# Performance work log

Hardware: AMD Instinct MI355X
Metric: run time of the kernel (lower is better)

Reference implementation:

```python
import jax, jax.numpy as jnp
import numpy as np

# Model dims
T0 = 2048      # tokens (batch*seq flattened)
D = 2048       # hidden_size
E = 256        # n_routed_experts
K = 8          # num_experts_per_tok
G = 8          # expert groups
EG = 32        # experts per group
R = 64         # tucker rank
I = 1408       # moe_intermediate_size


def setup_inputs() -> dict:
    key = jax.random.key(0)
    ks = jax.random.split(key, 12)
    f = lambda k, s: jax.random.normal(k, s, dtype=jnp.float32) * 0.02
    return {
        "hidden_states": jax.random.normal(ks[0], (T0, D), dtype=jnp.float32),
        "w_gate": f(ks[1], (D, E)),
        # Tucker factors per group: shared in-factor A, per-expert core C, shared out-factor B
        "A_gate": f(ks[2], (G, D, R)), "C_gate": f(ks[3], (G, EG, R, R)), "B_gate": f(ks[4], (G, R, I)),
        "A_up":   f(ks[5], (G, D, R)), "C_up":   f(ks[6], (G, EG, R, R)), "B_up":   f(ks[7], (G, R, I)),
        "A_down": f(ks[8], (G, I, R)), "C_down": f(ks[9], (G, EG, R, R)), "B_down": f(ks[10], (G, R, D)),
    }


def _tucker(x, A, C, B, inner):
    # x: [T, d_in], A: [d_in, R], C: [EG, R, R] gathered per-token, B: [R, d_out]
    h1 = x @ A                                    # [T, R]
    h2 = jnp.einsum('tr,trs->ts', h1, C[inner])   # per-token expert core
    return h2 @ B                                 # [T, d_out]


def reference(hidden_states, w_gate, A_gate, C_gate, B_gate,
              A_up, C_up, B_up, A_down, C_down, B_down):
    # Router: softmax in fp32, top-k, renormalize
    logits = hidden_states @ w_gate                              # [T0, E]
    probs = jax.nn.softmax(logits.astype(jnp.float32), axis=-1)
    rw, sel = jax.lax.top_k(probs, K)                            # [T0, K]
    rw = (rw / rw.sum(axis=-1, keepdims=True)).astype(hidden_states.dtype)

    idx = sel.reshape(-1)          # [T0*K] expert ids of dispatched rows
    gid = idx // EG                # group id
    inner = idx % EG               # expert within group
    x = jnp.repeat(hidden_states, K, axis=0)   # repeat_interleave dispatch [T0*K, D]

    out = jnp.zeros_like(x)
    for g in range(G):             # static loop over 8 structurally distinct groups
        m = (gid == g)[:, None]
        xg = jnp.where(m, x, 0.0)  # masked dispatch (zeros flow to zero through the MLP)
        go = _tucker(xg, A_gate[g], C_gate[g], B_gate[g], inner)
        uo = _tucker(xg, A_up[g],   C_up[g],   B_up[g],   inner)
        inter = jax.nn.silu(go) * uo
        do = _tucker(inter, A_down[g], C_down[g], B_down[g], inner)
        out = out + jnp.where(m, do, 0.0)

    # weighted combine
    return (out.reshape(T0, K, D) * rw[..., None]).sum(axis=1)
```

## Files before the change

kernel.cpp:

```cpp
#include <hip/hip_runtime.h>
#include <math.h>

constexpr int T0n = 2048;
constexpr int Dn  = 2048;
constexpr int En  = 256;
constexpr int Gn  = 8;
constexpr int EGn = 32;
constexpr int Rn  = 64;
constexpr int In  = 1408;

constexpr int NROWS = T0n * 8;
constexpr int SEGCAP = NROWS;
constexpr int KS_R = 6;
constexpr int NTILE2_MAX = NROWS / 256 + Gn;

typedef __attribute__((ext_vector_type(8))) short s8v;
typedef __attribute__((ext_vector_type(4))) float f4v;
typedef __attribute__((ext_vector_type(4))) int i4v;
#define MFMA16(a, b, c) __builtin_amdgcn_mfma_f32_16x16x32_bf16(a, b, c, 0, 0, 0)
#define MFMAI8(a, b, c) __builtin_amdgcn_mfma_i32_16x16x64_i8(a, b, c, 0, 0, 0)

__device__ __forceinline__ unsigned short f2bf(float x) {
  unsigned int u = __float_as_uint(x);
  unsigned int r = (u + 0x7FFFu + ((u >> 16) & 1u)) >> 16;
  return (unsigned short)r;
}

struct TD { const float* src; unsigned short* dst; int rows, cols, nbx, per_batch, base; };
struct TD9 { TD t[9]; };

__global__ __launch_bounds__(256) void k_tcvt9(TD9 D) {
  __shared__ float tbuf[32][33];
  int id = blockIdx.x;
  int ti = 0;
#pragma unroll
  for (int i = 1; i < 9; ++i) ti = (id >= D.t[i].base) ? i : ti;
  TD d = D.t[ti];
  int local = id - d.base;
  int bz = local / d.per_batch;
  int rem = local - bz * d.per_batch;
  int by = rem / d.nbx;
  int bx = rem - by * d.nbx;

  size_t boff = (size_t)bz * d.rows * d.cols;
  const float* src = d.src + boff;
  unsigned short* dst = d.dst + boff;
  int c0 = bx * 32, r0 = by * 32;
  int tx = threadIdx.x & 31, ty = threadIdx.x >> 5;
  for (int i = ty; i < 32; i += 8)
    tbuf[i][tx] = src[(size_t)(r0 + i) * d.cols + c0 + tx];
  __syncthreads();
  for (int i = ty; i < 32; i += 8)
    dst[(size_t)(c0 + i) * d.rows + r0 + tx] = f2bf(tbuf[tx][i]);
}

__global__ __launch_bounds__(256) void k_hcvt(
    const float* __restrict__ H, unsigned short* __restrict__ Hbf) {
  size_t i = ((size_t)blockIdx.x * 256 + threadIdx.x) * 8;
  float4 v0 = *(const float4*)&H[i];
  float4 v1 = *(const float4*)&H[i + 4];
  ushort4 o0, o1;
  o0.x = f2bf(v0.x); o0.y = f2bf(v0.y); o0.z = f2bf(v0.z); o0.w = f2bf(v0.w);
  o1.x = f2bf(v1.x); o1.y = f2bf(v1.y); o1.z = f2bf(v1.z); o1.w = f2bf(v1.w);
  *(ushort4*)&Hbf[i] = o0;
  *(ushort4*)&Hbf[i + 4] = o1;
}

__device__ __forceinline__ int4 limbs4(float v, double sc) {
  double d = (double)v * sc;
  d = fmin(fmax(d, -2.0e9), 2.0e9);
  int x = __double2int_rn(d);
  int l0 = (int)(signed char)(x & 0xff); x = (x - l0) >> 8;
  int l1 = (int)(signed char)(x & 0xff); x = (x - l1) >> 8;
  int l2 = (int)(signed char)(x & 0xff); x = (x - l2) >> 8;
  return make_int4(l0, l1, l2, x);
}

__global__ __launch_bounds__(256) void k_quant_h(
    const float* __restrict__ H, char* __restrict__ hq) {
  const size_t PL = (size_t)T0n * Dn;
  size_t i = (size_t)blockIdx.x * 256 + threadIdx.x;
  float4 v = *(const float4*)&H[i * 4];
  int4 a = limbs4(v.x, 268435456.0);
  int4 b = limbs4(v.y, 268435456.0);
  int4 c = limbs4(v.z, 268435456.0);
  int4 d = limbs4(v.w, 268435456.0);
  unsigned int p0 = (a.x & 0xff) | ((b.x & 0xff) << 8) | ((c.x & 0xff) << 16) | ((unsigned)(d.x & 0xff) << 24);
  unsigned int p1 = (a.y & 0xff) | ((b.y & 0xff) << 8) | ((c.y & 0xff) << 16) | ((unsigned)(d.y & 0xff) << 24);
  unsigned int p2 = (a.z & 0xff) | ((b.z & 0xff) << 8) | ((c.z & 0xff) << 16) | ((unsigned)(d.z & 0xff) << 24);
  unsigned int p3 = (a.w & 0xff) | ((b.w & 0xff) << 8) | ((c.w & 0xff) << 16) | ((unsigned)(d.w & 0xff) << 24);
  *(unsigned int*)&hq[0 * PL + i * 4] = p0;
  *(unsigned int*)&hq[1 * PL + i * 4] = p1;
  *(unsigned int*)&hq[2 * PL + i * 4] = p2;
  *(unsigned int*)&hq[3 * PL + i * 4] = p3;
}

__global__ __launch_bounds__(256) void k_quant_wT(
    const float* __restrict__ W, char* __restrict__ wqT) {
  __shared__ float tb[32][33];
  const size_t PL = (size_t)En * Dn;
  int kb = blockIdx.x * 32, nb = blockIdx.y * 32;
  int tx = threadIdx.x & 31, ty = threadIdx.x >> 5;
  for (int i = ty; i < 32; i += 8)
    tb[i][tx] = W[(size_t)(kb + i) * En + nb + tx];
  __syncthreads();
  for (int i = ty; i < 32; i += 8) {
    int4 l = limbs4(tb[tx][i], 8589934592.0);
    size_t off = (size_t)(nb + i) * Dn + kb + tx;
    wqT[0 * PL + off] = (char)l.x;
    wqT[1 * PL + off] = (char)l.y;
    wqT[2 * PL + off] = (char)l.z;
    wqT[3 * PL + off] = (char)l.w;
  }
}

__global__ __launch_bounds__(256) void k_router_i8(
    const char* __restrict__ hq, const char* __restrict__ wqT,
    float* __restrict__ part) {
  __shared__ __align__(16) char Asl[4][64][80];
  __shared__ __align__(16) char Bsl[4][64][80];
  const int n0 = blockIdx.x * 64, m0 = blockIdx.y * 64;
  const int kc = blockIdx.z;
  const int tid = threadIdx.x;
  const int w = tid >> 6, ln = tid & 63;
  const int quad = ln >> 4, lane16 = ln & 15;

  const char* ha = hq + ((size_t)w * T0n + m0 + ln) * Dn;
  const char* ba = wqT + ((size_t)w * En + n0 + ln) * Dn;

  i4v acc[4][4] = {};

  const int kbeg = ((kc * 32) / KS_R) * 64;
  const int kend = (((kc + 1) * 32) / KS_R) * 64;
  for (int k0 = kbeg; k0 < kend; k0 += 64) {
#pragma unroll
    for (int q = 0; q < 4; ++q) {
      *(uint4*)&Asl[w][ln][q * 16] = *(const uint4*)&ha[k0 + q * 16];
      *(uint4*)&Bsl[w][ln][q * 16] = *(const uint4*)&ba[k0 + q * 16];
    }
    __syncthreads();
    i4v b0 = *(const i4v*)&Bsl[0][w * 16 + lane16][quad * 16];
    i4v b1 = *(const i4v*)&Bsl[1][w * 16 + lane16][quad * 16];
    i4v b2 = *(const i4v*)&Bsl[2][w * 16 + lane16][quad * 16];
    i4v b3 = *(const i4v*)&Bsl[3][w * 16 + lane16][quad * 16];
#pragma unroll
    for (int mt = 0; mt < 4; ++mt) {
      i4v a0 = *(const i4v*)&Asl[0][mt * 16 + lane16][quad * 16];
      i4v a1 = *(const i4v*)&Asl[1][mt * 16 + lane16][quad * 16];
      i4v a2 = *(const i4v*)&Asl[2][mt * 16 + lane16][quad * 16];
      i4v a3 = *(const i4v*)&Asl[3][mt * 16 + lane16][quad * 16];
      acc[mt][0] = MFMAI8(a0, b3, acc[mt][0]);
      acc[mt][0] = MFMAI8(a1, b2, acc[mt][0]);
      acc[mt][0] = MFMAI8(a2, b1, acc[mt][0]);
      acc[mt][0] = MFMAI8(a3, b0, acc[mt][0]);
      acc[mt][1] = MFMAI8(a1, b3, acc[mt][1]);
      acc[mt][1] = MFMAI8(a2, b2, acc[mt][1]);
      acc[mt][1] = MFMAI8(a3, b1, acc[mt][1]);
      acc[mt][2] = MFMAI8(a2, b3, acc[mt][2]);
      acc[mt][2] = MFMAI8(a3, b2, acc[mt][2]);
      acc[mt][3] = MFMAI8(a3, b3, acc[mt][3]);
    }
    __syncthreads();
  }

  float* prow = part + (size_t)kc * T0n * En;
#pragma unroll
  for (int mt = 0; mt < 4; ++mt)
#pragma unroll
    for (int r = 0; r < 4; ++r) {
      int row = m0 + mt * 16 + quad * 4 + r;
      int col = n0 + w * 16 + lane16;
      double v = (double)acc[mt][0][r] * 0x1p-37 +
                 (double)acc[mt][1][r] * 0x1p-29 +
                 (double)acc[mt][2][r] * 0x1p-21 +
                 (double)acc[mt][3][r] * 0x1p-13;
      prow[(size_t)row * En + col] = (float)v;
    }
}

__global__ __launch_bounds__(256) void k_topk(
    const float* __restrict__ part, int* __restrict__ sel,
    float* __restrict__ rw, int* __restrict__ cnt_e) {
  const int wid = threadIdx.x >> 6, ln = threadIdx.x & 63;
  const int t = blockIdx.x * 4 + wid;

  double v[4];
#pragma unroll
  for (int j = 0; j < 4; ++j) {
    double s = 0.0;
#pragma unroll
    for (int kc = 0; kc < KS_R; ++kc)
      s += (double)part[((size_t)kc * T0n + t) * En + ln + 64 * j];
    v[j] = s;
  }

  float topv[8];
  int topi[8];
#pragma unroll
  for (int k = 0; k < 8; ++k) {
    double bv = v[0]; int bi = ln;
#pragma unroll
    for (int j = 1; j < 4; ++j) {
      int cand = ln + 64 * j;
      if (v[j] > bv || (v[j] == bv && cand < bi)) { bv = v[j]; bi = cand; }
    }
#pragma unroll
    for (int off = 32; off > 0; off >>= 1) {
      double ov = __shfl_xor(bv, off);
      int oi = __shfl_xor(bi, off);
      if (ov > bv || (ov == bv && oi < bi)) { bv = ov; bi = oi; }
    }
    topv[k] = (float)bv; topi[k] = bi;
    if ((bi & 63) == ln) v[bi >> 6] = -1e300;
  }

  if (ln < 8) {
    float m = topv[0];
    float ssum = 0.f;
#pragma unroll
    for (int k = 0; k < 8; ++k) ssum += expf(topv[k] - m);
    rw[t * 8 + ln] = expf(topv[ln] - m) / ssum;
    sel[t * 8 + ln] = topi[ln];
    atomicAdd(&cnt_e[topi[ln]], 1);
  }
}

__global__ __launch_bounds__(256) void k_scan(
    const int* __restrict__ cnt_e, int* __restrict__ off_e,
    int* __restrict__ cur_e, int* __restrict__ grp_n) {
  __shared__ int c[256];
  int tid = threadIdx.x;
  c[tid] = cnt_e[tid];
  __syncthreads();
  int g = tid >> 5, ei = tid & 31;
  int run = 0;
  for (int i = 0; i < ei; ++i) run += c[(g << 5) + i];
  off_e[tid] = g * SEGCAP + run;
  cur_e[tid] = g * SEGCAP + run;
  if (ei == 31) grp_n[g] = run + c[tid];
}

__global__ void k_scatter(const int* __restrict__ sel, int* __restrict__ cur_e,
                          int* __restrict__ rseg) {
  int i = blockIdx.x * 256 + threadIdx.x;
  int e = sel[i];
  int pos = atomicAdd(&cur_e[e], 1);
  rseg[pos] = i;
}

__global__ __launch_bounds__(512) void k_h1_mfma(
    const unsigned short* __restrict__ Hbf,
    const unsigned short* __restrict__ AgT, const unsigned short* __restrict__ AuT,
    unsigned short* __restrict__ h1gb, unsigned short* __restrict__ h1ub) {
  const int t0 = blockIdx.x * 64;
  const int g = blockIdx.y;
  const unsigned short* Wg = AgT + (size_t)g * Rn * Dn;
  const unsigned short* Wu = AuT + (size_t)g * Rn * Dn;

  __shared__ unsigned short As[64 * 72];
  __shared__ unsigned short Bg_l[64 * 72];
  __shared__ unsigned short Bu_l[64 * 72];
  const int tid = threadIdx.x;
  const int w = tid >> 6, ln = tid & 63;
  const int path = w >> 2, ws = w & 3;
  const int quad = ln >> 4, lane16 = ln & 15;
  const int j = tid >> 3, q = (tid & 7) * 8;

  f4v S[4] = {};

  uint4 sH, sG, sU;
  {
    sH = *(const uint4*)&Hbf[(size_t)(t0 + j) * Dn + q];
    sG = *(const uint4*)&Wg[(size_t)j * Dn + q];
    sU = *(const uint4*)&Wu[(size_t)j * Dn + q];
  }

  for (int k0 = 0; k0 < Dn; k0 += 64) {
    *(uint4*)&As[j * 72 + q] = sH;
    *(uint4*)&Bg_l[j * 72 + q] = sG;
    *(uint4*)&Bu_l[j * 72 + q] = sU;
    __syncthreads();

    if (k0 + 64 < Dn) {
      sH = *(const uint4*)&Hbf[(size_t)(t0 + j) * Dn + k0 + 64 + q];
      sG = *(const uint4*)&Wg[(size_t)j * Dn + k0 + 64 + q];
      sU = *(const uint4*)&Wu[(size_t)j * Dn + k0 + 64 + q];
    }

    const unsigned short* Bl = path ? Bu_l : Bg_l;
#pragma unroll
    for (int kk = 0; kk < 2; ++kk) {
      s8v a = *(const s8v*)&As[(ws * 16 + lane16) * 72 + kk * 32 + quad * 8];
#pragma unroll
      for (int nt = 0; nt < 4; ++nt) {
        s8v b = *(const s8v*)&Bl[(nt * 16 + lane16) * 72 + kk * 32 + quad * 8];
        S[nt] = MFMA16(a, b, S[nt]);
      }
    }
    __syncthreads();
  }
  unsigned short* out = path ? h1ub : h1gb;
#pragma unroll
  for (int nt = 0; nt < 4; ++nt)
#pragma unroll
    for (int r = 0; r < 4; ++r) {
      int row = t0 + ws * 16 + quad * 4 + r;
      int col = g * 64 + nt * 16 + lane16;
      out[(size_t)row * (Gn * Rn) + col] = f2bf(S[nt][r]);
    }
}

__global__ __launch_bounds__(512) void k_core_gu(
    const unsigned short* __restrict__ h1gb, const unsigned short* __restrict__ h1ub,
    const unsigned short* __restrict__ CgT, const unsigned short* __restrict__ CuT,
    const int* __restrict__ rseg, const int* __restrict__ off_e,
    const int* __restrict__ cnt_e,
    unsigned short* __restrict__ h2gb, unsigned short* __restrict__ h2ub) {
  const int e = blockIdx.x;
  const int ne = cnt_e[e];
  if (ne == 0) return;
  const int g = e >> 5;
  const int base = off_e[e];
  __shared__ unsigned short Cg_l[64 * 72];
  __shared__ unsigned short Cu_l[64 * 72];
  __shared__ unsigned short Ags[64 * 72];
  __shared__ unsigned short Aus[64 * 72];
  __shared__ int rids[64];
  const int tid = threadIdx.x;
  const int w = tid >> 6, ln = tid & 63;
  const int path = w >> 2, ws = w & 3;
  const int quad = ln >> 4, lane16 = ln & 15;
  const int j = tid >> 3, q = (tid & 7) * 8;
  {
    const unsigned short* cg = CgT + (size_t)e * (Rn * Rn);
    const unsigned short* cu = CuT + (size_t)e * (Rn * Rn);
    *(uint4*)&Cg_l[j * 72 + q] = *(const uint4*)&cg[j * 64 + q];
    *(uint4*)&Cu_l[j * 72 + q] = *(const uint4*)&cu[j * 64 + q];
  }
  const int ntile = (ne + 63) >> 6;
  for (int it = 0; it < ntile; ++it) {
    int mi = it * 64 + j;
    int rid = (mi < ne) ? rseg[base + mi] : -1;
    if ((tid & 7) == 0) rids[j] = rid;
    uint4 zg = {0, 0, 0, 0}, zu = {0, 0, 0, 0};
    if (rid >= 0) {
      zg = *(const uint4*)&h1gb[(size_t)(rid >> 3) * (Gn * Rn) + g * 64 + q];
      zu = *(const uint4*)&h1ub[(size_t)(rid >> 3) * (Gn * Rn) + g * 64 + q];
    }
    *(uint4*)&Ags[j * 72 + q] = zg;
    *(uint4*)&Aus[j * 72 + q] = zu;
    __syncthreads();
    const unsigned short* Al = path ? Aus : Ags;
    const unsigned short* Cl = path ? Cu_l : Cg_l;
    f4v S[4] = {};
#pragma unroll
    for (int kk = 0; kk < 2; ++kk) {
      s8v a = *(const s8v*)&Al[(ws * 16 + lane16) * 72 + kk * 32 + quad * 8];
#pragma unroll
      for (int nt = 0; nt < 4; ++nt) {
        s8v b = *(const s8v*)&Cl[(nt * 16 + lane16) * 72 + kk * 32 + quad * 8];
        S[nt] = MFMA16(a, b, S[nt]);
      }
    }
    unsigned short* out = path ? h2ub : h2gb;
#pragma unroll
    for (int nt = 0; nt < 4; ++nt)
#pragma unroll
      for (int r = 0; r < 4; ++r) {
        int rid2 = rids[ws * 16 + quad * 4 + r];
        if (rid2 >= 0)
          out[(size_t)rid2 * 64 + nt * 16 + lane16] = f2bf(S[nt][r]);
      }
    __syncthreads();
  }
}

__global__ __launch_bounds__(512) void k_expand_mfma(
    const unsigned short* __restrict__ h2gb, const unsigned short* __restrict__ h2ub,
    const unsigned short* __restrict__ BgT, const unsigned short* __restrict__ BuT,
    const unsigned short* __restrict__ AdT,
    const int* __restrict__ rseg, const int* __restrict__ grp_n,
    float* __restrict__ h1d) {
  int t = blockIdx.x;
  int g = -1, m0 = 0, ng = 0;
  {
    int pre = 0;
#pragma unroll
    for (int gg = 0; gg < Gn; ++gg) {
      int n = grp_n[gg];
      int nt = (n + 255) >> 8;
      if (g < 0 && t < pre + nt) { g = gg; m0 = (t - pre) << 8; ng = n; }
      pre += nt;
    }
  }
  if (g < 0) return;
  const int c_beg = blockIdx.y * 6;
  const int c_end = min(22, c_beg + 6);

  __shared__ unsigned short Bg_l[64 * 72];
  __shared__ unsigned short Bu_l[64 * 72];
  __shared__ unsigned short Ad_l[64 * 72];
  __shared__ unsigned short inter_l[8][32 * 72];
  __shared__ int rids[256];

  const int tid = threadIdx.x;
  const int w = tid >> 6, ln = tid & 63;
  const int quad = ln >> 4, lane16 = ln & 15;

  if (tid < 256) rids[tid] = (m0 + tid < ng) ? rseg[g * SEGCAP + m0 + tid] : -1;
  __syncthreads();

  s8v ag[2][2], au[2][2];
#pragma unroll
  for (int mt = 0; mt < 2; ++mt) {
    int rid = rids[w * 32 + mt * 16 + lane16];
#pragma unroll
    for (int kk = 0; kk < 2; ++kk) {
      s8v zg = {}, zu = {};
      if (rid >= 0) {
        zg = *(const s8v*)&h2gb[(size_t)rid * 64 + kk * 32 + quad * 8];
        zu = *(const s8v*)&h2ub[(size_t)rid * 64 + kk * 32 + quad * 8];
      }
      ag[mt][kk] = zg;
      au[mt][kk] = zu;
    }
  }

  const unsigned short* Bg_base = BgT + (size_t)g * In * Rn;
  const unsigned short* Bu_base = BuT + (size_t)g * In * Rn;
  const unsigned short* Ad_base = AdT + (size_t)g * Rn * In;

  unsigned short* ib = &inter_l[w][0];
  f4v P[2][4] = {};
  const int srow = tid >> 3, sco = (tid & 7) * 8;

  uint4 sg, su, sd;
  {
    const int i0 = c_beg * 64;
    sg = *(const uint4*)&Bg_base[(size_t)(i0 + srow) * Rn + sco];
    su = *(const uint4*)&Bu_base[(size_t)(i0 + srow) * Rn + sco];
    sd = *(const uint4*)&Ad_base[(size_t)srow * In + i0 + sco];
  }

  for (int c = c_beg; c < c_end; ++c) {
    *(uint4*)&Bg_l[srow * 72 + sco] = sg;
    *(uint4*)&Bu_l[srow * 72 + sco] = su;
    *(uint4*)&Ad_l[srow * 72 + sco] = sd;
    __syncthreads();

    if (c + 1 < c_end) {
      const int i1 = (c + 1) * 64;
      sg = *(const uint4*)&Bg_base[(size_t)(i1 + srow) * Rn + sco];
      su = *(const uint4*)&Bu_base[(size_t)(i1 + srow) * Rn + sco];
      sd = *(const uint4*)&Ad_base[(size_t)srow * In + i1 + sco];
    }

    f4v Sg[2][4] = {}, Su[2][4] = {};
#pragma unroll
    for (int kk = 0; kk < 2; ++kk) {
      s8v bg[4], bu[4];
#pragma unroll
      for (int nt = 0; nt < 4; ++nt) {
        bg[nt] = *(const s8v*)&Bg_l[(nt * 16 + lane16) * 72 + kk * 32 + quad * 8];
        bu[nt] = *(const s8v*)&Bu_l[(nt * 16 + lane16) * 72 + kk * 32 + quad * 8];
      }
#pragma unroll
      for (int mt = 0; mt < 2; ++mt)
#pragma unroll
        for (int nt = 0; nt < 4; ++nt) {
          Sg[mt][nt] = MFMA16(ag[mt][kk], bg[nt], Sg[mt][nt]);
          Su[mt][nt] = MFMA16(au[mt][kk], bu[nt], Su[mt][nt]);
        }
    }

#pragma unroll
    for (int mt = 0; mt < 2; ++mt)
#pragma unroll
      for (int nt = 0; nt < 4; ++nt)
#pragma unroll
        for (int r = 0; r < 4; ++r) {
          float sg2 = Sg[mt][nt][r];
          float v = sg2 / (1.f + __expf(-sg2)) * Su[mt][nt][r];
          ib[(mt * 16 + quad * 4 + r) * 72 + nt * 16 + lane16] = f2bf(v);
        }
    asm volatile("s_waitcnt lgkmcnt(0)" ::: "memory");

#pragma unroll
    for (int kk = 0; kk < 2; ++kk) {
      s8v ai[2], bd[4];
#pragma unroll
      for (int mt = 0; mt < 2; ++mt)
        ai[mt] = *(const s8v*)&ib[(mt * 16 + lane16) * 72 + kk * 32 + quad * 8];
#pragma unroll
      for (int nt = 0; nt < 4; ++nt)
        bd[nt] = *(const s8v*)&Ad_l[(nt * 16 + lane16) * 72 + kk * 32 + quad * 8];
#pragma unroll
      for (int mt = 0; mt < 2; ++mt)
#pragma unroll
        for (int nt = 0; nt < 4; ++nt)
          P[mt][nt] = MFMA16(ai[mt], bd[nt], P[mt][nt]);
    }
    __syncthreads();
  }

#pragma unroll
  for (int mt = 0; mt < 2; ++mt)
#pragma unroll
    for (int nt = 0; nt < 4; ++nt)
#pragma unroll
      for (int r = 0; r < 4; ++r) {
        int lrow = w * 32 + mt * 16 + quad * 4 + r;
        int rid = rids[lrow];
        if (rid >= 0)
          atomicAdd(&h1d[(size_t)rid * 64 + nt * 16 + lane16], P[mt][nt][r]);
      }
}

__global__ __launch_bounds__(512) void k_core_down(
    const float* __restrict__ h1d, const unsigned short* __restrict__ CdT,
    const float* __restrict__ rw,
    const int* __restrict__ rseg, const int* __restrict__ off_e,
    const int* __restrict__ cnt_e,
    float* __restrict__ y) {
  const int e = blockIdx.x;
  const int ne = cnt_e[e];
  if (ne == 0) return;
  const int g = e >> 5;
  const int base = off_e[e];
  __shared__ unsigned short Bd_l[64 * 72];
  __shared__ unsigned short Ad_l[128 * 72];
  __shared__ int rids[128];
  const int tid = threadIdx.x;
  const int w = tid >> 6, ln = tid & 63;
  const int quad = ln >> 4, lane16 = ln & 15;
  {
    int j = tid >> 3, q = (tid & 7) * 8;
    const unsigned short* cd = CdT + (size_t)e * (Rn * Rn);
    *(uint4*)&Bd_l[j * 72 + q] = *(const uint4*)&cd[j * 64 + q];
  }
  const int gj = tid >> 2, gq = (tid & 3) * 16;
  const int ntile = (ne + 127) >> 7;
  for (int it = 0; it < ntile; ++it) {
    int mi = it * 128 + gj;
    int rid = (mi < ne) ? rseg[base + mi] : -1;
    if ((tid & 3) == 0) rids[gj] = rid;
#pragma unroll
    for (int i = 0; i < 4; ++i) {
      int kb = gq + i * 4;
      float4 vd = {0.f, 0.f, 0.f, 0.f};
      if (rid >= 0) vd = *(const float4*)&h1d[(size_t)rid * 64 + kb];
      ushort4 od;
      od.x = f2bf(vd.x); od.y = f2bf(vd.y); od.z = f2bf(vd.z); od.w = f2bf(vd.w);
      *(ushort4*)&Ad_l[gj * 72 + kb] = od;
    }
    __syncthreads();
    f4v Sd[4] = {};
#pragma unroll
    for (int kk = 0; kk < 2; ++kk) {
      s8v ad = *(const s8v*)&Ad_l[(w * 16 + lane16) * 72 + kk * 32 + quad * 8];
#pragma unroll
      for (int nt = 0; nt < 4; ++nt) {
        s8v bd = *(const s8v*)&Bd_l[(nt * 16 + lane16) * 72 + kk * 32 + quad * 8];
        Sd[nt] = MFMA16(ad, bd, Sd[nt]);
      }
    }
#pragma unroll
    for (int nt = 0; nt < 4; ++nt)
#pragma unroll
      for (int r = 0; r < 4; ++r) {
        int rid2 = rids[w * 16 + quad * 4 + r];
        if (rid2 >= 0) {
          float wgt = rw[rid2];
          atomicAdd(&y[(size_t)(rid2 >> 3) * (Gn * Rn) + g * 64 + nt * 16 + lane16],
                    wgt * Sd[nt][r]);
        }
      }
    __syncthreads();
  }
}

__global__ __launch_bounds__(256) void k_combine(
    const float* __restrict__ y, const unsigned short* __restrict__ BdT,
    float* __restrict__ outp) {
  const int t0 = blockIdx.y * 128, n0 = blockIdx.x * 128;
  __shared__ unsigned short As[128 * 72];
  __shared__ unsigned short Bs[128 * 72];
  const int tid = threadIdx.x;
  const int w = tid >> 6, ln = tid & 63;
  const int quad = ln >> 4, lane16 = ln & 15;
  const int mbase = (w >> 1) * 64, nbase = (w & 1) * 64;

  f4v acc[4][4] = {};

  for (int k0 = 0; k0 < Gn * Rn; k0 += 64) {
#pragma unroll
    for (int i = 0; i < 8; ++i) {
      int c = tid + i * 256;
      int row = c >> 4, cc = (c & 15) * 4;
      float4 v = *(const float4*)&y[(size_t)(t0 + row) * (Gn * Rn) + k0 + cc];
      ushort4 o;
      o.x = f2bf(v.x); o.y = f2bf(v.y); o.z = f2bf(v.z); o.w = f2bf(v.w);
      *(ushort4*)&As[row * 72 + cc] = o;
    }
#pragma unroll
    for (int i = 0; i < 4; ++i) {
      int c = tid + i * 256;
      int row = c >> 3, cc = (c & 7) * 8;
      *(uint4*)&Bs[row * 72 + cc] = *(const uint4*)&BdT[(size_t)(n0 + row) * (Gn * Rn) + k0 + cc];
    }
    __syncthreads();
#pragma unroll
    for (int kk = 0; kk < 2; ++kk) {
      s8v a[4], b[4];
#pragma unroll
      for (int mt = 0; mt < 4; ++mt)
        a[mt] = *(const s8v*)&As[(mbase + mt * 16 + lane16) * 72 + kk * 32 + quad * 8];
#pragma unroll
      for (int nt = 0; nt < 4; ++nt)
        b[nt] = *(const s8v*)&Bs[(nbase + nt * 16 + lane16) * 72 + kk * 32 + quad * 8];
#pragma unroll
      for (int mt = 0; mt < 4; ++mt)
#pragma unroll
        for (int nt = 0; nt < 4; ++nt)
          acc[mt][nt] = MFMA16(a[mt], b[nt], acc[mt][nt]);
    }
    __syncthreads();
  }
#pragma unroll
  for (int mt = 0; mt < 4; ++mt)
#pragma unroll
    for (int nt = 0; nt < 4; ++nt)
#pragma unroll
      for (int r = 0; r < 4; ++r)
        outp[(size_t)(t0 + mbase + mt * 16 + quad * 4 + r) * Dn +
             n0 + nbase + nt * 16 + lane16] = acc[mt][nt][r];
}

extern "C" void kernel_launch(void* const* d_in, const int* in_sizes, int n_in,
                              void* d_out, int out_size, void* d_ws, size_t ws_size,
                              hipStream_t stream) {
  const float* hidden = (const float*)d_in[0];
  const float* w_gate = (const float*)d_in[1];
  const float* A_gate = (const float*)d_in[2];
  const float* C_gate = (const float*)d_in[3];
  const float* B_gate = (const float*)d_in[4];
  const float* A_up   = (const float*)d_in[5];
  const float* C_up   = (const float*)d_in[6];
  const float* B_up   = (const float*)d_in[7];
  const float* A_down = (const float*)d_in[8];
  const float* C_down = (const float*)d_in[9];
  const float* B_down = (const float*)d_in[10];
  float* out = (float*)d_out;

  char* base = (char*)d_ws;
  size_t o = 0;
  unsigned short* h2gb = (unsigned short*)(base + o); o += (size_t)NROWS * Rn * 2;
  unsigned short* h2ub = (unsigned short*)(base + o); o += (size_t)NROWS * Rn * 2;
  unsigned short* AgT  = (unsigned short*)(base + o); o += (size_t)Gn * Rn * Dn * 2;
  unsigned short* AuT  = (unsigned short*)(base + o); o += (size_t)Gn * Rn * Dn * 2;
  unsigned short* BgT  = (unsigned short*)(base + o); o += (size_t)Gn * In * Rn * 2;
  unsigned short* BuT  = (unsigned short*)(base + o); o += (size_t)Gn * In * Rn * 2;
  unsigned short* AdT  = (unsigned short*)(base + o); o += (size_t)Gn * Rn * In * 2;
  unsigned short* BdT  = (unsigned short*)(base + o); o += (size_t)Dn * Gn * Rn * 2;
  unsigned short* CgT  = (unsigned short*)(base + o); o += (size_t)En * Rn * Rn * 2;
  unsigned short* CuT  = (unsigned short*)(base + o); o += (size_t)En * Rn * Rn * 2;
  unsigned short* CdT  = (unsigned short*)(base + o); o += (size_t)En * Rn * Rn * 2;
  unsigned short* h1gb = (unsigned short*)(base + o); o += (size_t)T0n * Gn * Rn * 2;
  unsigned short* h1ub = (unsigned short*)(base + o); o += (size_t)T0n * Gn * Rn * 2;
  float* h1d = (float*)(base + o); o += (size_t)NROWS * Rn * 4;
  float* y   = (float*)(base + o); o += (size_t)T0n * Gn * Rn * 4;
  float* rwp = (float*)(base + o); o += (size_t)NROWS * 4;
  int* sel   = (int*)(base + o); o += (size_t)NROWS * 4;
  int* rseg  = (int*)(base + o); o += (size_t)Gn * SEGCAP * 4;
  int* cnt_e = (int*)(base + o); o += En * 4;
  int* off_e = (int*)(base + o); o += En * 4;
  int* cur_e = (int*)(base + o); o += En * 4;
  int* grp_n = (int*)(base + o); o += Gn * 4;
  float* part = (float*)base;
  char* hq  = base + (size_t)KS_R * T0n * En * 4;
  char* wqT = hq + (size_t)4 * T0n * Dn;
  unsigned short* Hbf = (unsigned short*)h1d;

  hipMemsetAsync(cnt_e, 0, En * sizeof(int), stream);

  k_quant_h<<<T0n * Dn / 1024, 256, 0, stream>>>(hidden, hq);
  k_quant_wT<<<dim3(Dn / 32, En / 32), 256, 0, stream>>>(w_gate, wqT);
  k_router_i8<<<dim3(En / 64, T0n / 64, KS_R), 256, 0, stream>>>(hq, wqT, part);
  k_topk<<<T0n / 4, 256, 0, stream>>>(part, sel, rwp, cnt_e);
  k_scan<<<1, 256, 0, stream>>>(cnt_e, off_e, cur_e, grp_n);
  k_scatter<<<NROWS / 256, 256, 0, stream>>>(sel, cur_e, rseg);

  k_hcvt<<<T0n * Dn / 2048, 256, 0, stream>>>(hidden, Hbf);

  {
    TD9 D;
    D.t[0] = {A_gate, AgT, Dn, Rn, Rn / 32, (Rn / 32) * (Dn / 32), 0};
    D.t[1] = {A_up,   AuT, Dn, Rn, Rn / 32, (Rn / 32) * (Dn / 32), 1024};
    D.t[2] = {B_gate, BgT, Rn, In, In / 32, (In / 32) * (Rn / 32), 2048};
    D.t[3] = {B_up,   BuT, Rn, In, In / 32, (In / 32) * (Rn / 32), 2752};
    D.t[4] = {A_down, AdT, In, Rn, Rn / 32, (Rn / 32) * (In / 32), 3456};
    D.t[5] = {B_down, BdT, Gn * Rn, Dn, Dn / 32, (Dn / 32) * (Gn * Rn / 32), 4160};
    D.t[6] = {C_gate, CgT, Rn, Rn, 2, 4, 5184};
    D.t[7] = {C_up,   CuT, Rn, Rn, 2, 4, 6208};
    D.t[8] = {C_down, CdT, Rn, Rn, 2, 4, 7232};
    k_tcvt9<<<8256, 256, 0, stream>>>(D);
  }

  k_h1_mfma<<<dim3(T0n / 64, Gn), 512, 0, stream>>>(Hbf, AgT, AuT, h1gb, h1ub);

  hipMemsetAsync(h1d, 0, (size_t)NROWS * Rn * sizeof(float), stream);
  hipMemsetAsync(y,   0, (size_t)T0n * Gn * Rn * sizeof(float), stream);

  k_core_gu<<<En, 512, 0, stream>>>(h1gb, h1ub, CgT, CuT,
                                    rseg, off_e, cnt_e, h2gb, h2ub);
  k_expand_mfma<<<dim3(NTILE2_MAX, 4), 512, 0, stream>>>(
      h2gb, h2ub, BgT, BuT, AdT, rseg, grp_n, h1d);
  k_core_down<<<En, 512, 0, stream>>>(h1d, CdT, rwp,
                                      rseg, off_e, cnt_e, y);
  k_combine<<<dim3(Dn / 128, T0n / 128), 256, 0, stream>>>(y, BdT, out);
}
```

Baseline: 290.0 us.

## Merge quant kernels, combine memsets, and register-prefetch combine GEMM with 512 threads

Merges the two router quantization kernels into one launch that branches on block index, and replaces two adjacent memsets (h1d and y are contiguous in the workspace) with one. The final combine GEMM moves to 512 threads with 8 waves, each computing a 64x32 sub-tile. It also prefetches the next K-slice of y and BdT into registers while the MFMAs run on the current one. The aim is to cut launch overhead and hide global-load latency in the combine step, at the cost of higher register use and a contiguity assumption for the merged memset.

```diff
diff --git a/kernel.cpp b/kernel.cpp
--- a/kernel.cpp
+++ b/kernel.cpp
@@ -76,41 +76,43 @@
   return make_int4(l0, l1, l2, x);
 }
 
-__global__ __launch_bounds__(256) void k_quant_h(
-    const float* __restrict__ H, char* __restrict__ hq) {
-  const size_t PL = (size_t)T0n * Dn;
-  size_t i = (size_t)blockIdx.x * 256 + threadIdx.x;
-  float4 v = *(const float4*)&H[i * 4];
-  int4 a = limbs4(v.x, 268435456.0);
-  int4 b = limbs4(v.y, 268435456.0);
-  int4 c = limbs4(v.z, 268435456.0);
-  int4 d = limbs4(v.w, 268435456.0);
-  unsigned int p0 = (a.x & 0xff) | ((b.x & 0xff) << 8) | ((c.x & 0xff) << 16) | ((unsigned)(d.x & 0xff) << 24);
-  unsigned int p1 = (a.y & 0xff) | ((b.y & 0xff) << 8) | ((c.y & 0xff) << 16) | ((unsigned)(d.y & 0xff) << 24);
-  unsigned int p2 = (a.z & 0xff) | ((b.z & 0xff) << 8) | ((c.z & 0xff) << 16) | ((unsigned)(d.z & 0xff) << 24);
-  unsigned int p3 = (a.w & 0xff) | ((b.w & 0xff) << 8) | ((c.w & 0xff) << 16) | ((unsigned)(d.w & 0xff) << 24);
-  *(unsigned int*)&hq[0 * PL + i * 4] = p0;
-  *(unsigned int*)&hq[1 * PL + i * 4] = p1;
-  *(unsigned int*)&hq[2 * PL + i * 4] = p2;
-  *(unsigned int*)&hq[3 * PL + i * 4] = p3;
-}
-
-__global__ __launch_bounds__(256) void k_quant_wT(
-    const float* __restrict__ W, char* __restrict__ wqT) {
+__global__ __launch_bounds__(256) void k_quant(
+    const float* __restrict__ H, const float* __restrict__ W,
+    char* __restrict__ hq, char* __restrict__ wqT) {
   __shared__ float tb[32][33];
-  const size_t PL = (size_t)En * Dn;
-  int kb = blockIdx.x * 32, nb = blockIdx.y * 32;
-  int tx = threadIdx.x & 31, ty = threadIdx.x >> 5;
-  for (int i = ty; i < 32; i += 8)
-    tb[i][tx] = W[(size_t)(kb + i) * En + nb + tx];
-  __syncthreads();
-  for (int i = ty; i < 32; i += 8) {
-    int4 l = limbs4(tb[tx][i], 8589934592.0);
-    size_t off = (size_t)(nb + i) * Dn + kb + tx;
-    wqT[0 * PL + off] = (char)l.x;
-    wqT[1 * PL + off] = (char)l.y;
-    wqT[2 * PL + off] = (char)l.z;
-    wqT[3 * PL + off] = (char)l.w;
+  const int id = blockIdx.x;
+  if (id < 4096) {
+    const size_t PL = (size_t)T0n * Dn;
+    size_t i = (size_t)id * 256 + threadIdx.x;
+    float4 v = *(const float4*)&H[i * 4];
+    int4 a = limbs4(v.x, 268435456.0);
+    int4 b = limbs4(v.y, 268435456.0);
+    int4 c = limbs4(v.z, 268435456.0);
+    int4 d = limbs4(v.w, 268435456.0);
+    unsigned int p0 = (a.x & 0xff) | ((b.x & 0xff) << 8) | ((c.x & 0xff) << 16) | ((unsigned)(d.x & 0xff) << 24);
+    unsigned int p1 = (a.y & 0xff) | ((b.y & 0xff) << 8) | ((c.y & 0xff) << 16) | ((unsigned)(d.y & 0xff) << 24);
+    unsigned int p2 = (a.z & 0xff) | ((b.z & 0xff) << 8) | ((c.z & 0xff) << 16) | ((unsigned)(d.z & 0xff) << 24);
+    unsigned int p3 = (a.w & 0xff) | ((b.w & 0xff) << 8) | ((c.w & 0xff) << 16) | ((unsigned)(d.w & 0xff) << 24);
+    *(unsigned int*)&hq[0 * PL + i * 4] = p0;
+    *(unsigned int*)&hq[1 * PL + i * 4] = p1;
+    *(unsigned int*)&hq[2 * PL + i * 4] = p2;
+    *(unsigned int*)&hq[3 * PL + i * 4] = p3;
+  } else {
+    const size_t PL = (size_t)En * Dn;
+    int local = id - 4096;
+    int kb = (local & 63) * 32, nb = (local >> 6) * 32;
+    int tx = threadIdx.x & 31, ty = threadIdx.x >> 5;
+    for (int i = ty; i < 32; i += 8)
+      tb[i][tx] = W[(size_t)(kb + i) * En + nb + tx];
+    __syncthreads();
+    for (int i = ty; i < 32; i += 8) {
+      int4 l = limbs4(tb[tx][i], 8589934592.0);
+      size_t off = (size_t)(nb + i) * Dn + kb + tx;
+      wqT[0 * PL + off] = (char)l.x;
+      wqT[1 * PL + off] = (char)l.y;
+      wqT[2 * PL + off] = (char)l.z;
+      wqT[3 * PL + off] = (char)l.w;
+    }
   }
 }
 
@@ -579,7 +581,7 @@
   }
 }
 
-__global__ __launch_bounds__(256) void k_combine(
+__global__ __launch_bounds__(512) void k_combine(
     const float* __restrict__ y, const unsigned short* __restrict__ BdT,
     float* __restrict__ outp) {
   const int t0 = blockIdx.y * 128, n0 = blockIdx.x * 128;
@@ -588,40 +590,71 @@
   const int tid = threadIdx.x;
   const int w = tid >> 6, ln = tid & 63;
   const int quad = ln >> 4, lane16 = ln & 15;
-  const int mbase = (w >> 1) * 64, nbase = (w & 1) * 64;
-
-  f4v acc[4][4] = {};
+  const int mbase = (w >> 2) * 64, nbase = (w & 3) * 32;
+
+  f4v acc[4][2] = {};
+
+  float4 sy[4];
+  uint4 sb[2];
+#pragma unroll
+  for (int i = 0; i < 4; ++i) {
+    int c = tid + i * 512;
+    int row = c >> 4, cc = (c & 15) * 4;
+    sy[i] = *(const float4*)&y[(size_t)(t0 + row) * (Gn * Rn) + cc];
+  }
+#pragma unroll
+  for (int i = 0; i < 2; ++i) {
+    int c = tid + i * 512;
+    int row = c >> 3, cc = (c & 7) * 8;
+    sb[i] = *(const uint4*)&BdT[(size_t)(n0 + row) * (Gn * Rn) + cc];
+  }
 
   for (int k0 = 0; k0 < Gn * Rn; k0 += 64) {
 #pragma unroll
-    for (int i = 0; i < 8; ++i) {
-      int c = tid + i * 256;
+    for (int i = 0; i < 4; ++i) {
+      int c = tid + i * 512;
       int row = c >> 4, cc = (c & 15) * 4;
-      float4 v = *(const float4*)&y[(size_t)(t0 + row) * (Gn * Rn) + k0 + cc];
       ushort4 o;
-      o.x = f2bf(v.x); o.y = f2bf(v.y); o.z = f2bf(v.z); o.w = f2bf(v.w);
+      o.x = f2bf(sy[i].x); o.y = f2bf(sy[i].y);
+      o.z = f2bf(sy[i].z); o.w = f2bf(sy[i].w);
       *(ushort4*)&As[row * 72 + cc] = o;
     }
 #pragma unroll
-    for (int i = 0; i < 4; ++i) {
-      int c = tid + i * 256;
+    for (int i = 0; i < 2; ++i) {
+      int c = tid + i * 512;
       int row = c >> 3, cc = (c & 7) * 8;
-      *(uint4*)&Bs[row * 72 + cc] = *(const uint4*)&BdT[(size_t)(n0 + row) * (Gn * Rn) + k0 + cc];
-    }
-    __syncthreads();
+      *(uint4*)&Bs[row * 72 + cc] = sb[i];
+    }
+    __syncthreads();
+
+    if (k0 + 64 < Gn * Rn) {
+#pragma unroll
+      for (int i = 0; i < 4; ++i) {
+        int c = tid + i * 512;
+        int row = c >> 4, cc = (c & 15) * 4;
+        sy[i] = *(const float4*)&y[(size_t)(t0 + row) * (Gn * Rn) + k0 + 64 + cc];
+      }
+#pragma unroll
+      for (int i = 0; i < 2; ++i) {
+        int c = tid + i * 512;
+        int row = c >> 3, cc = (c & 7) * 8;
+        sb[i] = *(const uint4*)&BdT[(size_t)(n0 + row) * (Gn * Rn) + k0 + 64 + cc];
+      }
+    }
+
 #pragma unroll
     for (int kk = 0; kk < 2; ++kk) {
-      s8v a[4], b[4];
+      s8v a[4], b[2];
 #pragma unroll
       for (int mt = 0; mt < 4; ++mt)
         a[mt] = *(const s8v*)&As[(mbase + mt * 16 + lane16) * 72 + kk * 32 + quad * 8];
 #pragma unroll
-      for (int nt = 0; nt < 4; ++nt)
+      for (int nt = 0; nt < 2; ++nt)
         b[nt] = *(const s8v*)&Bs[(nbase + nt * 16 + lane16) * 72 + kk * 32 + quad * 8];
 #pragma unroll
       for (int mt = 0; mt < 4; ++mt)
 #pragma unroll
-        for (int nt = 0; nt < 4; ++nt)
+        for (int nt = 0; nt < 2; ++nt)
           acc[mt][nt] = MFMA16(a[mt], b[nt], acc[mt][nt]);
     }
     __syncthreads();
@@ -629,7 +662,7 @@
 #pragma unroll
   for (int mt = 0; mt < 4; ++mt)
 #pragma unroll
-    for (int nt = 0; nt < 4; ++nt)
+    for (int nt = 0; nt < 2; ++nt)
 #pragma unroll
       for (int r = 0; r < 4; ++r)
         outp[(size_t)(t0 + mbase + mt * 16 + quad * 4 + r) * Dn +
@@ -683,8 +716,8 @@
 
   hipMemsetAsync(cnt_e, 0, En * sizeof(int), stream);
 
-  k_quant_h<<<T0n * Dn / 1024, 256, 0, stream>>>(hidden, hq);
-  k_quant_wT<<<dim3(Dn / 32, En / 32), 256, 0, stream>>>(w_gate, wqT);
+  k_quant<<<T0n * Dn / 1024 + (Dn / 32) * (En / 32), 256, 0, stream>>>(
+      hidden, w_gate, hq, wqT);
   k_router_i8<<<dim3(En / 64, T0n / 64, KS_R), 256, 0, stream>>>(hq, wqT, part);
   k_topk<<<T0n / 4, 256, 0, stream>>>(part, sel, rwp, cnt_e);
   k_scan<<<1, 256, 0, stream>>>(cnt_e, off_e, cur_e, grp_n);
@@ -708,8 +741,8 @@
 
   k_h1_mfma<<<dim3(T0n / 64, Gn), 512, 0, stream>>>(Hbf, AgT, AuT, h1gb, h1ub);
 
-  hipMemsetAsync(h1d, 0, (size_t)NROWS * Rn * sizeof(float), stream);
-  hipMemsetAsync(y,   0, (size_t)T0n * Gn * Rn * sizeof(float), stream);
+  hipMemsetAsync(h1d, 0, (size_t)(NROWS * Rn + T0n * Gn * Rn) * sizeof(float),
+                 stream);
 
   k_core_gu<<<En, 512, 0, stream>>>(h1gb, h1ub, CgT, CuT,
                                     rseg, off_e, cnt_e, h2gb, h2ub);
@@ -717,5 +750,5 @@
       h2gb, h2ub, BgT, BuT, AdT, rseg, grp_n, h1d);
   k_core_down<<<En, 512, 0, stream>>>(h1d, CdT, rwp,
                                       rseg, off_e, cnt_e, y);
-  k_combine<<<dim3(Dn / 128, T0n / 128), 256, 0, stream>>>(y, BdT, out);
-}
+  k_combine<<<dim3(Dn / 128, T0n / 128), 512, 0, stream>>>(y, BdT, out);
+}
```

New measurement: 288.7 us, median of 2. No clear change (-0.5%).
